# Kernel optimization log

Hardware: AMD Instinct MI355X
Metric: run time of the kernel (lower is better)

## Reference

```python
import jax, jax.numpy as jnp
import numpy as np

S, B, C, H, E = 4096, 2, 256, 8, 131072
CC = C // H


def setup_inputs() -> dict:
    key = jax.random.key(0)
    ks = jax.random.split(key, 12)
    sc = 0.02
    inp = {
        "x": jax.random.normal(ks[0], (S, B, C), jnp.float32),
        "q_id": jax.random.randint(ks[1], (E,), 0, S, jnp.int32),
        "k_id": jax.random.randint(ks[2], (E,), 0, S, jnp.int32),
        "Wq": jax.random.normal(ks[3], (C, C), jnp.float32) * sc,
        "bq": jnp.zeros((C,), jnp.float32),
        "Wk": jax.random.normal(ks[4], (C, C), jnp.float32) * sc,
        "bk": jnp.zeros((C,), jnp.float32),
        "Wv": jax.random.normal(ks[5], (C, C), jnp.float32) * sc,
        "bv": jnp.zeros((C,), jnp.float32),
        "Wx": jax.random.normal(ks[6], (C, C), jnp.float32) * sc,
        "bx": jnp.zeros((C,), jnp.float32),
    }
    return inp


def reference(x, q_id, k_id, Wq, bq, Wk, bk, Wv, bv, Wx, bx):
    s, b, c = x.shape
    cc = c // H
    # qkv projections (torch Linear: x @ W.T + b)
    q = (x @ Wq.T + bq).reshape(s, b, H, cc)
    k = (x @ Wk.T + bk).reshape(s, b, H, cc)
    v = (x @ Wv.T + bv).reshape(s, b, H, cc)
    # per-edge scores: gather along sequence axis by edge ids
    qk = jnp.einsum('ebhc,ebhc->ebh', q[q_id], k[k_id])[..., None]  # [E,b,h,1]
    qk = qk / jnp.sqrt(jnp.asarray(cc, x.dtype))
    eqk = jnp.exp(qk - jnp.max(qk))  # global max, as in original
    # scatter-add softmax normalizer and weighted sum over edges
    d = jnp.zeros((s, b, H, 1), x.dtype).at[q_id].add(eqk)
    out = jnp.zeros((s, b, H, cc), x.dtype).at[q_id].add(eqk * v[k_id])
    out = (out / d).reshape(s, b, c)
    return out @ Wx.T + bx
```

## Files before the change

### kernel.cpp

```cpp
#include <hip/hip_runtime.h>

constexpr int S_  = 4096;
constexpr int B_  = 2;
constexpr int C_  = 256;
constexpr int H_  = 8;
constexpr int E_  = 131072;
constexpr int CC_ = 32;
constexpr int MR  = S_ * B_;

typedef __attribute__((ext_vector_type(8))) short bf16x8_t;
typedef __attribute__((ext_vector_type(4))) float f32x4_t;

__device__ __forceinline__ unsigned short f2bf(float f) {
    unsigned int u = __float_as_uint(f);
    u += 0x7fffu + ((u >> 16) & 1u);
    return (unsigned short)(u >> 16);
}
__device__ __forceinline__ float bflo(unsigned int u) { return __uint_as_float(u << 16); }
__device__ __forceinline__ float bfhi(unsigned int u) { return __uint_as_float(u & 0xffff0000u); }

__device__ __forceinline__ void cast8(const float* __restrict__ src, unsigned short* __restrict__ dst, int i) {
    const float4* s = (const float4*)src + (size_t)i * 2;
    float4 a = s[0], b = s[1];
    uint4 o;
    o.x = (unsigned)f2bf(a.x) | ((unsigned)f2bf(a.y) << 16);
    o.y = (unsigned)f2bf(a.z) | ((unsigned)f2bf(a.w) << 16);
    o.z = (unsigned)f2bf(b.x) | ((unsigned)f2bf(b.y) << 16);
    o.w = (unsigned)f2bf(b.z) | ((unsigned)f2bf(b.w) << 16);
    *((uint4*)dst + i) = o;
}


__global__ __launch_bounds__(256) void prep_kernel(
        const int* __restrict__ q_id, int* __restrict__ count,
        const float* __restrict__ x, unsigned short* __restrict__ xb,
        const float* __restrict__ Wq, const float* __restrict__ Wk,
        const float* __restrict__ Wv, const float* __restrict__ Wx,
        unsigned short* __restrict__ Wb) {
    const int bid = blockIdx.x, tid = threadIdx.x;
    if (bid < 512) {
        atomicAdd(&count[q_id[bid * 256 + tid]], 1);
    } else if (bid < 1536) {
        cast8(x, xb, (bid - 512) * 256 + tid);
    } else {
        int idx = bid - 1536;
        int z = idx >> 5;
        const float* src = (z == 0) ? Wq : (z == 1) ? Wk : (z == 2) ? Wv : Wx;
        cast8(src, Wb + (size_t)z * (C_ * C_), (idx & 31) * 256 + tid);
    }
}


__global__ __launch_bounds__(1024) void scan_kernel(const int* __restrict__ count,
                                                    int* __restrict__ base,
                                                    int* __restrict__ cursor) {
    __shared__ int wsums[16];
    const int t = threadIdx.x, lane = t & 63, w = t >> 6;
    int c0 = count[4 * t + 0], c1 = count[4 * t + 1];
    int c2 = count[4 * t + 2], c3 = count[4 * t + 3];
    int tsum = c0 + c1 + c2 + c3;
    int x = tsum;
#pragma unroll
    for (int off = 1; off < 64; off <<= 1) {
        int y = __shfl_up(x, off);
        if (lane >= off) x += y;
    }
    if (lane == 63) wsums[w] = x;
    __syncthreads();
    if (t == 0) {
        int run = 0;
#pragma unroll
        for (int i = 0; i < 16; ++i) { int v = wsums[i]; wsums[i] = run; run += v; }
        base[S_] = run;
    }
    __syncthreads();
    int excl = x - tsum + wsums[w];
    int b0 = excl, b1 = b0 + c0, b2 = b1 + c1, b3 = b2 + c2;
    base[4 * t + 0] = b0; base[4 * t + 1] = b1;
    base[4 * t + 2] = b2; base[4 * t + 3] = b3;
    cursor[4 * t + 0] = b0; cursor[4 * t + 1] = b1;
    cursor[4 * t + 2] = b2; cursor[4 * t + 3] = b3;
}


__global__ __launch_bounds__(256) void scatter_qkv_kernel(
        const int* __restrict__ q_id, const int* __restrict__ k_id,
        int* __restrict__ cursor, int* __restrict__ koff_sorted,
        const unsigned short* __restrict__ xb, const unsigned short* __restrict__ Wb,
        const float* __restrict__ bq, const float* __restrict__ bk, const float* __restrict__ bv,
        unsigned short* __restrict__ qb, unsigned short* __restrict__ kvb) {
    __shared__ __align__(16) unsigned short As[64][264];
    const int bid = blockIdx.x, tid = threadIdx.x;
    if (bid >= 512) {
        int e = (bid - 512) * 256 + tid;
        int pos = atomicAdd(&cursor[q_id[e]], 1);
        koff_sorted[pos] = k_id[e] << 10;
        return;
    }
    const int nb = bid & 3, mg = bid >> 2;
    const int lane = tid & 63, wave = tid >> 6;
    const int l16 = lane & 15, quad = lane >> 4;
    const int colz = (nb << 6) + (wave << 4);

    bf16x8_t breg[3][8];
#pragma unroll
    for (int z = 0; z < 3; ++z) {
        const unsigned short* Wrow = Wb + (size_t)z * (C_ * C_) + (size_t)(colz + l16) * C_;
#pragma unroll
        for (int ks = 0; ks < 8; ++ks)
            breg[z][ks] = *(const bf16x8_t*)(Wrow + ks * 32 + quad * 8);
    }
    const float bc0 = bq[colz + l16];
    const float bc1 = bk[colz + l16];
    const float bc2 = bv[colz + l16];

    const int mbase = mg * 64;
#pragma unroll
    for (int it = 0; it < 8; ++it) {
        int l = it * 256 + tid;
        int r = l >> 5, cc = (l & 31) << 3;
        *(uint4*)&As[r][cc] = *(const uint4*)&xb[(size_t)(mbase + r) * C_ + cc];
    }
    __syncthreads();

#pragma unroll
    for (int mt = 0; mt < 4; ++mt) {
        bf16x8_t a[8];
#pragma unroll
        for (int ks = 0; ks < 8; ++ks)
            a[ks] = *(const bf16x8_t*)&As[mt * 16 + l16][ks * 32 + quad * 8];
        const int row0 = mbase + mt * 16 + quad * 4;
        {
            f32x4_t acc = {0.f, 0.f, 0.f, 0.f};
#pragma unroll
            for (int ks = 0; ks < 8; ++ks)
                acc = __builtin_amdgcn_mfma_f32_16x16x32_bf16(a[ks], breg[0][ks], acc, 0, 0, 0);
#pragma unroll
            for (int r = 0; r < 4; ++r)
                qb[(size_t)(row0 + r) * 256 + colz + l16] = f2bf(acc[r] + bc0);
        }
        {
            f32x4_t acc = {0.f, 0.f, 0.f, 0.f};
#pragma unroll
            for (int ks = 0; ks < 8; ++ks)
                acc = __builtin_amdgcn_mfma_f32_16x16x32_bf16(a[ks], breg[1][ks], acc, 0, 0, 0);
#pragma unroll
            for (int r = 0; r < 4; ++r)
                kvb[(size_t)(row0 + r) * 512 + colz + l16] = f2bf(acc[r] + bc1);
        }
        {
            f32x4_t acc = {0.f, 0.f, 0.f, 0.f};
#pragma unroll
            for (int ks = 0; ks < 8; ++ks)
                acc = __builtin_amdgcn_mfma_f32_16x16x32_bf16(a[ks], breg[2][ks], acc, 0, 0, 0);
#pragma unroll
            for (int r = 0; r < 4; ++r)
                kvb[(size_t)(row0 + r) * 512 + 256 + colz + l16] = f2bf(acc[r] + bc2);
        }
    }
}


__global__ __launch_bounds__(256) void attn_edge(
        const unsigned short* __restrict__ qb, const unsigned short* __restrict__ kvb,
        const int* __restrict__ base, const int* __restrict__ koff,
        unsigned short* __restrict__ attnb) {
    __shared__ float red[2][64][9];
    const int lane = threadIdx.x & 63;
    const int wave = threadIdx.x >> 6;
    const int rw = wave >> 1, part = wave & 1;
    const int s = blockIdx.x * 2 + rw;
    const int half = lane >> 5, hl = lane & 31;
    const int e0 = __builtin_amdgcn_readfirstlane(base[s]);
    const int e1 = __builtin_amdgcn_readfirstlane(base[s + 1]);

    const uint4 qq = *((const uint4*)(qb + (size_t)(s * 2 + half) * C_) + hl);
    const float q0 = bflo(qq.x), q1 = bfhi(qq.x), q2 = bflo(qq.y), q3 = bfhi(qq.y);
    const float q4 = bflo(qq.z), q5 = bfhi(qq.z), q6 = bflo(qq.w), q7 = bfhi(qq.w);

    float a0 = 0.f, a1 = 0.f, a2 = 0.f, a3 = 0.f, a4 = 0.f, a5 = 0.f, a6 = 0.f, a7 = 0.f;
    float wsum = 0.f;
    const float scale = 0.17677669529663687f;

    auto edge = [&](const uint4& kk, const uint4& vv) {
        float p = q0 * bflo(kk.x) + q1 * bfhi(kk.x)
                + q2 * bflo(kk.y) + q3 * bfhi(kk.y)
                + q4 * bflo(kk.z) + q5 * bfhi(kk.z)
                + q6 * bflo(kk.w) + q7 * bfhi(kk.w);
        p += __shfl_xor(p, 1);
        p += __shfl_xor(p, 2);
        const float w = __expf(p * scale);
        a0 = fmaf(w, bflo(vv.x), a0); a1 = fmaf(w, bfhi(vv.x), a1);
        a2 = fmaf(w, bflo(vv.y), a2); a3 = fmaf(w, bfhi(vv.y), a3);
        a4 = fmaf(w, bflo(vv.z), a4); a5 = fmaf(w, bfhi(vv.z), a5);
        a6 = fmaf(w, bflo(vv.w), a6); a7 = fmaf(w, bfhi(vv.w), a7);
        wsum += w;
    };
    auto fetch = [&](int my, int t, uint4& kk, uint4& vv) {
        int o = __builtin_amdgcn_readlane(my, part + 2 * t);
        const uint4* p = (const uint4*)(kvb + o + half * 512);
        kk = p[hl]; vv = p[32 + hl];
    };

    for (int b0 = e0; b0 < e1; b0 += 64) {
        const int m = min(64, e1 - b0);
        const int my = koff[b0 + ((lane < m) ? lane : 0)];
        const int nm = (m > part) ? ((m - part + 1) >> 1) : 0;
        uint4 k0 = {}, v0 = {}, k1 = {}, v1 = {};
        uint4 k2 = {}, v2 = {}, k3 = {}, v3 = {};
        if (nm > 0) fetch(my, 0, k0, v0);
        if (nm > 1) fetch(my, 1, k1, v1);
        if (nm > 2) fetch(my, 2, k2, v2);
        if (nm > 3) fetch(my, 3, k3, v3);
        int t = 0;
        for (; t + 7 < nm; t += 4) {
            edge(k0, v0); fetch(my, t + 4, k0, v0);
            edge(k1, v1); fetch(my, t + 5, k1, v1);
            edge(k2, v2); fetch(my, t + 6, k2, v2);
            edge(k3, v3); fetch(my, t + 7, k3, v3);
        }
        const int rem = nm - t;
        if (rem > 0) { edge(k0, v0); if (rem > 4) fetch(my, t + 4, k0, v0); }
        if (rem > 1) { edge(k1, v1); if (rem > 5) fetch(my, t + 5, k1, v1); }
        if (rem > 2) { edge(k2, v2); if (rem > 6) fetch(my, t + 6, k2, v2); }
        if (rem > 3) edge(k3, v3);
        if (rem > 4) edge(k0, v0);
        if (rem > 5) edge(k1, v1);
        if (rem > 6) edge(k2, v2);
    }

    if (part == 1) {
        float* r = red[rw][lane];
        r[0] = a0; r[1] = a1; r[2] = a2; r[3] = a3;
        r[4] = a4; r[5] = a5; r[6] = a6; r[7] = a7; r[8] = wsum;
    }
    __syncthreads();
    if (part == 0) {
        const float* r = red[rw][lane];
        a0 += r[0]; a1 += r[1]; a2 += r[2]; a3 += r[3];
        a4 += r[4]; a5 += r[5]; a6 += r[6]; a7 += r[7]; wsum += r[8];
        const float inv = 1.0f / wsum;
        uint4 o;
        o.x = (unsigned)f2bf(a0 * inv) | ((unsigned)f2bf(a1 * inv) << 16);
        o.y = (unsigned)f2bf(a2 * inv) | ((unsigned)f2bf(a3 * inv) << 16);
        o.z = (unsigned)f2bf(a4 * inv) | ((unsigned)f2bf(a5 * inv) << 16);
        o.w = (unsigned)f2bf(a6 * inv) | ((unsigned)f2bf(a7 * inv) << 16);
        *((uint4*)(attnb + (size_t)(s * 2 + half) * C_) + hl) = o;
    }
}


__global__ __launch_bounds__(256) void gemm_proj(
        const unsigned short* __restrict__ attnb, const unsigned short* __restrict__ Wxb,
        const float* __restrict__ bx, float* __restrict__ out) {
    __shared__ __align__(16) unsigned short As[64][264];
    const int tid = threadIdx.x;
    const int nb = blockIdx.x & 3, mg = blockIdx.x >> 2;
    const int lane = tid & 63, wave = tid >> 6;
    const int l16 = lane & 15, quad = lane >> 4;
    const int colz = (nb << 6) + (wave << 4);

    const unsigned short* Wrow = Wxb + (size_t)(colz + l16) * C_;
    bf16x8_t breg[8];
#pragma unroll
    for (int ks = 0; ks < 8; ++ks)
        breg[ks] = *(const bf16x8_t*)(Wrow + ks * 32 + quad * 8);
    const float bcol = bx[colz + l16];
    const int ocol = colz + l16;

    const int mbase = mg * 64;
#pragma unroll
    for (int it = 0; it < 8; ++it) {
        int l = it * 256 + tid;
        int r = l >> 5, cc = (l & 31) << 3;
        *(uint4*)&As[r][cc] = *(const uint4*)&attnb[(size_t)(mbase + r) * C_ + cc];
    }
    __syncthreads();
#pragma unroll
    for (int mt = 0; mt < 4; ++mt) {
        f32x4_t acc = {0.f, 0.f, 0.f, 0.f};
#pragma unroll
        for (int ks = 0; ks < 8; ++ks) {
            bf16x8_t a = *(const bf16x8_t*)&As[mt * 16 + l16][ks * 32 + quad * 8];
            acc = __builtin_amdgcn_mfma_f32_16x16x32_bf16(a, breg[ks], acc, 0, 0, 0);
        }
        const int row0 = mbase + mt * 16 + quad * 4;
#pragma unroll
        for (int r = 0; r < 4; ++r)
            out[(size_t)(row0 + r) * C_ + ocol] = acc[r] + bcol;
    }
}


extern "C" void kernel_launch(void* const* d_in, const int* in_sizes, int n_in,
                              void* d_out, int out_size, void* d_ws, size_t ws_size,
                              hipStream_t stream) {
    const float* x  = (const float*)d_in[0];
    const int* q_id = (const int*)d_in[1];
    const int* k_id = (const int*)d_in[2];
    const float* Wq = (const float*)d_in[3];
    const float* bq = (const float*)d_in[4];
    const float* Wk = (const float*)d_in[5];
    const float* bk = (const float*)d_in[6];
    const float* Wv = (const float*)d_in[7];
    const float* bv = (const float*)d_in[8];
    const float* Wx = (const float*)d_in[9];
    const float* bx = (const float*)d_in[10];
    float* out = (float*)d_out;

    char* ws = (char*)d_ws;
    unsigned short* xb    = (unsigned short*)ws;                 ws += (size_t)MR * C_ * 2;
    unsigned short* qb    = (unsigned short*)ws;                 ws += (size_t)MR * C_ * 2;
    unsigned short* kvb   = (unsigned short*)ws;                 ws += (size_t)MR * 512 * 2;
    unsigned short* attnb = (unsigned short*)ws;                 ws += (size_t)MR * C_ * 2;
    unsigned short* Wb    = (unsigned short*)ws;                 ws += (size_t)4 * C_ * C_ * 2;
    int* count       = (int*)ws;                                 ws += S_ * 4;
    int* base        = (int*)ws;                                 ws += (S_ + 1) * 4;
    int* cursor      = (int*)ws;                                 ws += S_ * 4;
    int* koff_sorted = (int*)ws;

    hipMemsetAsync(count, 0, S_ * sizeof(int), stream);
    prep_kernel<<<1664, 256, 0, stream>>>(q_id, count, x, xb, Wq, Wk, Wv, Wx, Wb);
    scan_kernel<<<1, 1024, 0, stream>>>(count, base, cursor);
    scatter_qkv_kernel<<<1024, 256, 0, stream>>>(q_id, k_id, cursor, koff_sorted,
                                                 xb, Wb, bq, bk, bv, qb, kvb);
    attn_edge<<<S_ / 2, 256, 0, stream>>>(qb, kvb, base, koff_sorted, attnb);
    gemm_proj<<<512, 256, 0, stream>>>(attnb, Wb + (size_t)3 * C_ * C_, bx, out);
}
```

Before: 145.0 us.

## Fuse all stages into one persistent kernel with software grid barriers

Replaces the five separate kernel launches (prep, scan, scatter+QKV GEMM, edge attention, output projection) with a single 512-block persistent kernel that separates phases with atomic-counter grid barriers. The aim is to remove launch gaps and per-kernel tail effects between the short stages. The attention phase also changes from two waves splitting each row's edges and reducing through shared memory to one wave per row. The design depends on all 512 blocks being co-resident (launch bounds allow 2 blocks per CU), and each phase has less parallelism than before, with the single-wave-per-row attention possibly lengthening the critical path.

```diff
diff --git a/kernel.cpp b/kernel.cpp
--- a/kernel.cpp
+++ b/kernel.cpp
@@ -5,8 +5,8 @@
 constexpr int C_  = 256;
 constexpr int H_  = 8;
 constexpr int E_  = 131072;
-constexpr int CC_ = 32;
 constexpr int MR  = S_ * B_;
+constexpr int NB  = 512;
 
 typedef __attribute__((ext_vector_type(8))) short bf16x8_t;
 typedef __attribute__((ext_vector_type(4))) float f32x4_t;
@@ -30,264 +30,233 @@
     *((uint4*)dst + i) = o;
 }
 
-
-__global__ __launch_bounds__(256) void prep_kernel(
-        const int* __restrict__ q_id, int* __restrict__ count,
-        const float* __restrict__ x, unsigned short* __restrict__ xb,
-        const float* __restrict__ Wq, const float* __restrict__ Wk,
-        const float* __restrict__ Wv, const float* __restrict__ Wx,
-        unsigned short* __restrict__ Wb) {
-    const int bid = blockIdx.x, tid = threadIdx.x;
-    if (bid < 512) {
-        atomicAdd(&count[q_id[bid * 256 + tid]], 1);
-    } else if (bid < 1536) {
-        cast8(x, xb, (bid - 512) * 256 + tid);
-    } else {
-        int idx = bid - 1536;
-        int z = idx >> 5;
-        const float* src = (z == 0) ? Wq : (z == 1) ? Wk : (z == 2) ? Wv : Wx;
-        cast8(src, Wb + (size_t)z * (C_ * C_), (idx & 31) * 256 + tid);
-    }
-}
-
-
-__global__ __launch_bounds__(1024) void scan_kernel(const int* __restrict__ count,
-                                                    int* __restrict__ base,
-                                                    int* __restrict__ cursor) {
-    __shared__ int wsums[16];
-    const int t = threadIdx.x, lane = t & 63, w = t >> 6;
-    int c0 = count[4 * t + 0], c1 = count[4 * t + 1];
-    int c2 = count[4 * t + 2], c3 = count[4 * t + 3];
-    int tsum = c0 + c1 + c2 + c3;
-    int x = tsum;
-#pragma unroll
-    for (int off = 1; off < 64; off <<= 1) {
-        int y = __shfl_up(x, off);
-        if (lane >= off) x += y;
-    }
-    if (lane == 63) wsums[w] = x;
+__device__ __forceinline__ void gbar(int* bar, int target) {
     __syncthreads();
-    if (t == 0) {
-        int run = 0;
-#pragma unroll
-        for (int i = 0; i < 16; ++i) { int v = wsums[i]; wsums[i] = run; run += v; }
-        base[S_] = run;
+    if (threadIdx.x == 0) {
+        __threadfence();
+        atomicAdd(bar, 1);
+        while (atomicAdd(bar, 0) < target)
+            __builtin_amdgcn_s_sleep(2);
+        __threadfence();
     }
     __syncthreads();
-    int excl = x - tsum + wsums[w];
-    int b0 = excl, b1 = b0 + c0, b2 = b1 + c1, b3 = b2 + c2;
-    base[4 * t + 0] = b0; base[4 * t + 1] = b1;
-    base[4 * t + 2] = b2; base[4 * t + 3] = b3;
-    cursor[4 * t + 0] = b0; cursor[4 * t + 1] = b1;
-    cursor[4 * t + 2] = b2; cursor[4 * t + 3] = b3;
-}
-
-
-__global__ __launch_bounds__(256) void scatter_qkv_kernel(
-        const int* __restrict__ q_id, const int* __restrict__ k_id,
-        int* __restrict__ cursor, int* __restrict__ koff_sorted,
-        const unsigned short* __restrict__ xb, const unsigned short* __restrict__ Wb,
-        const float* __restrict__ bq, const float* __restrict__ bk, const float* __restrict__ bv,
-        unsigned short* __restrict__ qb, unsigned short* __restrict__ kvb) {
+}
+
+__global__ __launch_bounds__(256, 2) void fused_kernel(
+        const float* __restrict__ x, const int* __restrict__ q_id, const int* __restrict__ k_id,
+        const float* __restrict__ Wq, const float* __restrict__ bq,
+        const float* __restrict__ Wk, const float* __restrict__ bk,
+        const float* __restrict__ Wv, const float* __restrict__ bv,
+        const float* __restrict__ Wx, const float* __restrict__ bx,
+        unsigned short* __restrict__ xb, unsigned short* __restrict__ qb,
+        unsigned short* __restrict__ kvb, unsigned short* __restrict__ attnb,
+        unsigned short* __restrict__ Wb,
+        int* __restrict__ count, int* bar, int* __restrict__ base,
+        int* __restrict__ cursor, int* __restrict__ koff,
+        float* __restrict__ out) {
     __shared__ __align__(16) unsigned short As[64][264];
     const int bid = blockIdx.x, tid = threadIdx.x;
-    if (bid >= 512) {
-        int e = (bid - 512) * 256 + tid;
-        int pos = atomicAdd(&cursor[q_id[e]], 1);
-        koff_sorted[pos] = k_id[e] << 10;
-        return;
-    }
-    const int nb = bid & 3, mg = bid >> 2;
+    const int gid = bid * 256 + tid;
     const int lane = tid & 63, wave = tid >> 6;
     const int l16 = lane & 15, quad = lane >> 4;
-    const int colz = (nb << 6) + (wave << 4);
-
-    bf16x8_t breg[3][8];
-#pragma unroll
-    for (int z = 0; z < 3; ++z) {
-        const unsigned short* Wrow = Wb + (size_t)z * (C_ * C_) + (size_t)(colz + l16) * C_;
+
+    cast8(x, xb, gid);
+    cast8(x, xb, gid + 131072);
+    if (gid < 32768) {
+        int z = gid >> 13, i = gid & 8191;
+        const float* src = (z == 0) ? Wq : (z == 1) ? Wk : (z == 2) ? Wv : Wx;
+        cast8(src, Wb + (size_t)z * (C_ * C_), i);
+    }
+    atomicAdd(&count[q_id[gid]], 1);
+    gbar(bar, NB);
+
+    if (bid == 0) {
+        const int4* cp = (const int4*)count;
+        int4 c0 = cp[tid * 4 + 0], c1 = cp[tid * 4 + 1];
+        int4 c2 = cp[tid * 4 + 2], c3 = cp[tid * 4 + 3];
+        int tsum = c0.x + c0.y + c0.z + c0.w + c1.x + c1.y + c1.z + c1.w
+                 + c2.x + c2.y + c2.z + c2.w + c3.x + c3.y + c3.z + c3.w;
+        int incl = tsum;
+        const int w = tid >> 6;
+#pragma unroll
+        for (int off = 1; off < 64; off <<= 1) {
+            int y = __shfl_up(incl, off);
+            if (lane >= off) incl += y;
+        }
+        int* wsums = (int*)As;
+        if (lane == 63) wsums[w] = incl;
+        __syncthreads();
+        int ws0 = wsums[0], ws1 = wsums[1], ws2 = wsums[2], ws3 = wsums[3];
+        __syncthreads();
+        if (tid == 0) base[S_] = ws0 + ws1 + ws2 + ws3;
+        int woff = (w > 0 ? ws0 : 0) + (w > 1 ? ws1 : 0) + (w > 2 ? ws2 : 0);
+        int run = woff + incl - tsum;
+        int idx = tid * 16;
+#define EMIT(V) { base[idx] = run; cursor[idx] = run; run += (V); ++idx; }
+        EMIT(c0.x) EMIT(c0.y) EMIT(c0.z) EMIT(c0.w)
+        EMIT(c1.x) EMIT(c1.y) EMIT(c1.z) EMIT(c1.w)
+        EMIT(c2.x) EMIT(c2.y) EMIT(c2.z) EMIT(c2.w)
+        EMIT(c3.x) EMIT(c3.y) EMIT(c3.z) EMIT(c3.w)
+#undef EMIT
+    }
+    for (int u = bid; u < 1024; u += NB) {
+        const int nb = u & 3, mg = u >> 2;
+        const int mbase = mg * 32;
+        __syncthreads();
+#pragma unroll
+        for (int it = 0; it < 4; ++it) {
+            int l = it * 256 + tid;
+            int r = l >> 5, cc = (l & 31) << 3;
+            *(uint4*)&As[r][cc] = *(const uint4*)&xb[(size_t)(mbase + r) * C_ + cc];
+        }
+        __syncthreads();
+        const int colz = (nb << 6) + (wave << 4);
+#pragma unroll
+        for (int z = 0; z < 3; ++z) {
+            const unsigned short* Wrow = Wb + (size_t)z * (C_ * C_) + (size_t)(colz + l16) * C_;
+            bf16x8_t breg[8];
+#pragma unroll
+            for (int ks = 0; ks < 8; ++ks)
+                breg[ks] = *(const bf16x8_t*)(Wrow + ks * 32 + quad * 8);
+            const float* bias = (z == 0) ? bq : (z == 1) ? bk : bv;
+            const float bcol = bias[colz + l16];
+#pragma unroll
+            for (int mt = 0; mt < 2; ++mt) {
+                f32x4_t acc = {0.f, 0.f, 0.f, 0.f};
+#pragma unroll
+                for (int ks = 0; ks < 8; ++ks) {
+                    bf16x8_t a = *(const bf16x8_t*)&As[mt * 16 + l16][ks * 32 + quad * 8];
+                    acc = __builtin_amdgcn_mfma_f32_16x16x32_bf16(a, breg[ks], acc, 0, 0, 0);
+                }
+                const int row0 = mbase + mt * 16 + quad * 4;
+                if (z == 0) {
+#pragma unroll
+                    for (int r = 0; r < 4; ++r)
+                        qb[(size_t)(row0 + r) * 256 + colz + l16] = f2bf(acc[r] + bcol);
+                } else if (z == 1) {
+#pragma unroll
+                    for (int r = 0; r < 4; ++r)
+                        kvb[(size_t)(row0 + r) * 512 + colz + l16] = f2bf(acc[r] + bcol);
+                } else {
+#pragma unroll
+                    for (int r = 0; r < 4; ++r)
+                        kvb[(size_t)(row0 + r) * 512 + 256 + colz + l16] = f2bf(acc[r] + bcol);
+                }
+            }
+        }
+    }
+    gbar(bar, 2 * NB);
+
+    {
+        int pos = atomicAdd(&cursor[q_id[gid]], 1);
+        koff[pos] = k_id[gid] << 10;
+    }
+    gbar(bar, 3 * NB);
+
+    {
+        const int half = lane >> 5, hl = lane & 31;
+        const float scale = 0.17677669529663687f;
+#pragma unroll
+        for (int it = 0; it < 2; ++it) {
+            const int s = (bid << 3) + (it << 2) + wave;
+            const int e0 = __builtin_amdgcn_readfirstlane(base[s]);
+            const int e1 = __builtin_amdgcn_readfirstlane(base[s + 1]);
+
+            const uint4 qq = *((const uint4*)(qb + (size_t)(s * 2 + half) * C_) + hl);
+            const float q0 = bflo(qq.x), q1 = bfhi(qq.x), q2 = bflo(qq.y), q3 = bfhi(qq.y);
+            const float q4 = bflo(qq.z), q5 = bfhi(qq.z), q6 = bflo(qq.w), q7 = bfhi(qq.w);
+
+            float a0 = 0.f, a1 = 0.f, a2 = 0.f, a3 = 0.f;
+            float a4 = 0.f, a5 = 0.f, a6 = 0.f, a7 = 0.f;
+            float wsum = 0.f;
+
+            auto edge = [&](const uint4& kk, const uint4& vv) {
+                float p = q0 * bflo(kk.x) + q1 * bfhi(kk.x)
+                        + q2 * bflo(kk.y) + q3 * bfhi(kk.y)
+                        + q4 * bflo(kk.z) + q5 * bfhi(kk.z)
+                        + q6 * bflo(kk.w) + q7 * bfhi(kk.w);
+                p += __shfl_xor(p, 1);
+                p += __shfl_xor(p, 2);
+                const float w = __expf(p * scale);
+                a0 = fmaf(w, bflo(vv.x), a0); a1 = fmaf(w, bfhi(vv.x), a1);
+                a2 = fmaf(w, bflo(vv.y), a2); a3 = fmaf(w, bfhi(vv.y), a3);
+                a4 = fmaf(w, bflo(vv.z), a4); a5 = fmaf(w, bfhi(vv.z), a5);
+                a6 = fmaf(w, bflo(vv.w), a6); a7 = fmaf(w, bfhi(vv.w), a7);
+                wsum += w;
+            };
+            auto fetch = [&](int my, int t, uint4& kk, uint4& vv) {
+                int o = __builtin_amdgcn_readlane(my, t);
+                const uint4* p = (const uint4*)(kvb + o + half * 512);
+                kk = p[hl]; vv = p[32 + hl];
+            };
+
+            for (int b0 = e0; b0 < e1; b0 += 64) {
+                const int m = min(64, e1 - b0);
+                const int my = koff[b0 + ((lane < m) ? lane : 0)];
+                uint4 k0 = {}, v0 = {}, k1 = {}, v1 = {};
+                uint4 k2 = {}, v2 = {}, k3 = {}, v3 = {};
+                if (m > 0) fetch(my, 0, k0, v0);
+                if (m > 1) fetch(my, 1, k1, v1);
+                if (m > 2) fetch(my, 2, k2, v2);
+                if (m > 3) fetch(my, 3, k3, v3);
+                int t = 0;
+                for (; t + 7 < m; t += 4) {
+                    edge(k0, v0); fetch(my, t + 4, k0, v0);
+                    edge(k1, v1); fetch(my, t + 5, k1, v1);
+                    edge(k2, v2); fetch(my, t + 6, k2, v2);
+                    edge(k3, v3); fetch(my, t + 7, k3, v3);
+                }
+                const int rem = m - t;
+                if (rem > 0) { edge(k0, v0); if (rem > 4) fetch(my, t + 4, k0, v0); }
+                if (rem > 1) { edge(k1, v1); if (rem > 5) fetch(my, t + 5, k1, v1); }
+                if (rem > 2) { edge(k2, v2); if (rem > 6) fetch(my, t + 6, k2, v2); }
+                if (rem > 3) edge(k3, v3);
+                if (rem > 4) edge(k0, v0);
+                if (rem > 5) edge(k1, v1);
+                if (rem > 6) edge(k2, v2);
+            }
+
+            const float inv = 1.0f / wsum;
+            uint4 o;
+            o.x = (unsigned)f2bf(a0 * inv) | ((unsigned)f2bf(a1 * inv) << 16);
+            o.y = (unsigned)f2bf(a2 * inv) | ((unsigned)f2bf(a3 * inv) << 16);
+            o.z = (unsigned)f2bf(a4 * inv) | ((unsigned)f2bf(a5 * inv) << 16);
+            o.w = (unsigned)f2bf(a6 * inv) | ((unsigned)f2bf(a7 * inv) << 16);
+            *((uint4*)(attnb + (size_t)(s * 2 + half) * C_) + hl) = o;
+        }
+    }
+    gbar(bar, 4 * NB);
+
+    {
+        const int nbp = bid & 3, mgp = bid >> 2;
+        const int mbase = mgp * 64;
+#pragma unroll
+        for (int it = 0; it < 8; ++it) {
+            int l = it * 256 + tid;
+            int r = l >> 5, cc = (l & 31) << 3;
+            *(uint4*)&As[r][cc] = *(const uint4*)&attnb[(size_t)(mbase + r) * C_ + cc];
+        }
+        __syncthreads();
+        const int colz = (nbp << 6) + (wave << 4);
+        const unsigned short* Wrow = Wb + (size_t)3 * (C_ * C_) + (size_t)(colz + l16) * C_;
+        bf16x8_t breg[8];
 #pragma unroll
         for (int ks = 0; ks < 8; ++ks)
-            breg[z][ks] = *(const bf16x8_t*)(Wrow + ks * 32 + quad * 8);
-    }
-    const float bc0 = bq[colz + l16];
-    const float bc1 = bk[colz + l16];
-    const float bc2 = bv[colz + l16];
-
-    const int mbase = mg * 64;
-#pragma unroll
-    for (int it = 0; it < 8; ++it) {
-        int l = it * 256 + tid;
-        int r = l >> 5, cc = (l & 31) << 3;
-        *(uint4*)&As[r][cc] = *(const uint4*)&xb[(size_t)(mbase + r) * C_ + cc];
-    }
-    __syncthreads();
-
-#pragma unroll
-    for (int mt = 0; mt < 4; ++mt) {
-        bf16x8_t a[8];
-#pragma unroll
-        for (int ks = 0; ks < 8; ++ks)
-            a[ks] = *(const bf16x8_t*)&As[mt * 16 + l16][ks * 32 + quad * 8];
-        const int row0 = mbase + mt * 16 + quad * 4;
-        {
+            breg[ks] = *(const bf16x8_t*)(Wrow + ks * 32 + quad * 8);
+        const float bcol = bx[colz + l16];
+#pragma unroll
+        for (int mt = 0; mt < 4; ++mt) {
             f32x4_t acc = {0.f, 0.f, 0.f, 0.f};
 #pragma unroll
-            for (int ks = 0; ks < 8; ++ks)
-                acc = __builtin_amdgcn_mfma_f32_16x16x32_bf16(a[ks], breg[0][ks], acc, 0, 0, 0);
+            for (int ks = 0; ks < 8; ++ks) {
+                bf16x8_t a = *(const bf16x8_t*)&As[mt * 16 + l16][ks * 32 + quad * 8];
+                acc = __builtin_amdgcn_mfma_f32_16x16x32_bf16(a, breg[ks], acc, 0, 0, 0);
+            }
+            const int row0 = mbase + mt * 16 + quad * 4;
 #pragma unroll
             for (int r = 0; r < 4; ++r)
-                qb[(size_t)(row0 + r) * 256 + colz + l16] = f2bf(acc[r] + bc0);
-        }
-        {
-            f32x4_t acc = {0.f, 0.f, 0.f, 0.f};
-#pragma unroll
-            for (int ks = 0; ks < 8; ++ks)
-                acc = __builtin_amdgcn_mfma_f32_16x16x32_bf16(a[ks], breg[1][ks], acc, 0, 0, 0);
-#pragma unroll
-            for (int r = 0; r < 4; ++r)
-                kvb[(size_t)(row0 + r) * 512 + colz + l16] = f2bf(acc[r] + bc1);
-        }
-        {
-            f32x4_t acc = {0.f, 0.f, 0.f, 0.f};
-#pragma unroll
-            for (int ks = 0; ks < 8; ++ks)
-                acc = __builtin_amdgcn_mfma_f32_16x16x32_bf16(a[ks], breg[2][ks], acc, 0, 0, 0);
-#pragma unroll
-            for (int r = 0; r < 4; ++r)
-                kvb[(size_t)(row0 + r) * 512 + 256 + colz + l16] = f2bf(acc[r] + bc2);
-        }
-    }
-}
-
-
-__global__ __launch_bounds__(256) void attn_edge(
-        const unsigned short* __restrict__ qb, const unsigned short* __restrict__ kvb,
-        const int* __restrict__ base, const int* __restrict__ koff,
-        unsigned short* __restrict__ attnb) {
-    __shared__ float red[2][64][9];
-    const int lane = threadIdx.x & 63;
-    const int wave = threadIdx.x >> 6;
-    const int rw = wave >> 1, part = wave & 1;
-    const int s = blockIdx.x * 2 + rw;
-    const int half = lane >> 5, hl = lane & 31;
-    const int e0 = __builtin_amdgcn_readfirstlane(base[s]);
-    const int e1 = __builtin_amdgcn_readfirstlane(base[s + 1]);
-
-    const uint4 qq = *((const uint4*)(qb + (size_t)(s * 2 + half) * C_) + hl);
-    const float q0 = bflo(qq.x), q1 = bfhi(qq.x), q2 = bflo(qq.y), q3 = bfhi(qq.y);
-    const float q4 = bflo(qq.z), q5 = bfhi(qq.z), q6 = bflo(qq.w), q7 = bfhi(qq.w);
-
-    float a0 = 0.f, a1 = 0.f, a2 = 0.f, a3 = 0.f, a4 = 0.f, a5 = 0.f, a6 = 0.f, a7 = 0.f;
-    float wsum = 0.f;
-    const float scale = 0.17677669529663687f;
-
-    auto edge = [&](const uint4& kk, const uint4& vv) {
-        float p = q0 * bflo(kk.x) + q1 * bfhi(kk.x)
-                + q2 * bflo(kk.y) + q3 * bfhi(kk.y)
-                + q4 * bflo(kk.z) + q5 * bfhi(kk.z)
-                + q6 * bflo(kk.w) + q7 * bfhi(kk.w);
-        p += __shfl_xor(p, 1);
-        p += __shfl_xor(p, 2);
-        const float w = __expf(p * scale);
-        a0 = fmaf(w, bflo(vv.x), a0); a1 = fmaf(w, bfhi(vv.x), a1);
-        a2 = fmaf(w, bflo(vv.y), a2); a3 = fmaf(w, bfhi(vv.y), a3);
-        a4 = fmaf(w, bflo(vv.z), a4); a5 = fmaf(w, bfhi(vv.z), a5);
-        a6 = fmaf(w, bflo(vv.w), a6); a7 = fmaf(w, bfhi(vv.w), a7);
-        wsum += w;
-    };
-    auto fetch = [&](int my, int t, uint4& kk, uint4& vv) {
-        int o = __builtin_amdgcn_readlane(my, part + 2 * t);
-        const uint4* p = (const uint4*)(kvb + o + half * 512);
-        kk = p[hl]; vv = p[32 + hl];
-    };
-
-    for (int b0 = e0; b0 < e1; b0 += 64) {
-        const int m = min(64, e1 - b0);
-        const int my = koff[b0 + ((lane < m) ? lane : 0)];
-        const int nm = (m > part) ? ((m - part + 1) >> 1) : 0;
-        uint4 k0 = {}, v0 = {}, k1 = {}, v1 = {};
-        uint4 k2 = {}, v2 = {}, k3 = {}, v3 = {};
-        if (nm > 0) fetch(my, 0, k0, v0);
-        if (nm > 1) fetch(my, 1, k1, v1);
-        if (nm > 2) fetch(my, 2, k2, v2);
-        if (nm > 3) fetch(my, 3, k3, v3);
-        int t = 0;
-        for (; t + 7 < nm; t += 4) {
-            edge(k0, v0); fetch(my, t + 4, k0, v0);
-            edge(k1, v1); fetch(my, t + 5, k1, v1);
-            edge(k2, v2); fetch(my, t + 6, k2, v2);
-            edge(k3, v3); fetch(my, t + 7, k3, v3);
-        }
-        const int rem = nm - t;
-        if (rem > 0) { edge(k0, v0); if (rem > 4) fetch(my, t + 4, k0, v0); }
-        if (rem > 1) { edge(k1, v1); if (rem > 5) fetch(my, t + 5, k1, v1); }
-        if (rem > 2) { edge(k2, v2); if (rem > 6) fetch(my, t + 6, k2, v2); }
-        if (rem > 3) edge(k3, v3);
-        if (rem > 4) edge(k0, v0);
-        if (rem > 5) edge(k1, v1);
-        if (rem > 6) edge(k2, v2);
-    }
-
-    if (part == 1) {
-        float* r = red[rw][lane];
-        r[0] = a0; r[1] = a1; r[2] = a2; r[3] = a3;
-        r[4] = a4; r[5] = a5; r[6] = a6; r[7] = a7; r[8] = wsum;
-    }
-    __syncthreads();
-    if (part == 0) {
-        const float* r = red[rw][lane];
-        a0 += r[0]; a1 += r[1]; a2 += r[2]; a3 += r[3];
-        a4 += r[4]; a5 += r[5]; a6 += r[6]; a7 += r[7]; wsum += r[8];
-        const float inv = 1.0f / wsum;
-        uint4 o;
-        o.x = (unsigned)f2bf(a0 * inv) | ((unsigned)f2bf(a1 * inv) << 16);
-        o.y = (unsigned)f2bf(a2 * inv) | ((unsigned)f2bf(a3 * inv) << 16);
-        o.z = (unsigned)f2bf(a4 * inv) | ((unsigned)f2bf(a5 * inv) << 16);
-        o.w = (unsigned)f2bf(a6 * inv) | ((unsigned)f2bf(a7 * inv) << 16);
-        *((uint4*)(attnb + (size_t)(s * 2 + half) * C_) + hl) = o;
-    }
-}
-
-
-__global__ __launch_bounds__(256) void gemm_proj(
-        const unsigned short* __restrict__ attnb, const unsigned short* __restrict__ Wxb,
-        const float* __restrict__ bx, float* __restrict__ out) {
-    __shared__ __align__(16) unsigned short As[64][264];
-    const int tid = threadIdx.x;
-    const int nb = blockIdx.x & 3, mg = blockIdx.x >> 2;
-    const int lane = tid & 63, wave = tid >> 6;
-    const int l16 = lane & 15, quad = lane >> 4;
-    const int colz = (nb << 6) + (wave << 4);
-
-    const unsigned short* Wrow = Wxb + (size_t)(colz + l16) * C_;
-    bf16x8_t breg[8];
-#pragma unroll
-    for (int ks = 0; ks < 8; ++ks)
-        breg[ks] = *(const bf16x8_t*)(Wrow + ks * 32 + quad * 8);
-    const float bcol = bx[colz + l16];
-    const int ocol = colz + l16;
-
-    const int mbase = mg * 64;
-#pragma unroll
-    for (int it = 0; it < 8; ++it) {
-        int l = it * 256 + tid;
-        int r = l >> 5, cc = (l & 31) << 3;
-        *(uint4*)&As[r][cc] = *(const uint4*)&attnb[(size_t)(mbase + r) * C_ + cc];
-    }
-    __syncthreads();
-#pragma unroll
-    for (int mt = 0; mt < 4; ++mt) {
-        f32x4_t acc = {0.f, 0.f, 0.f, 0.f};
-#pragma unroll
-        for (int ks = 0; ks < 8; ++ks) {
-            bf16x8_t a = *(const bf16x8_t*)&As[mt * 16 + l16][ks * 32 + quad * 8];
-            acc = __builtin_amdgcn_mfma_f32_16x16x32_bf16(a, breg[ks], acc, 0, 0, 0);
-        }
-        const int row0 = mbase + mt * 16 + quad * 4;
-#pragma unroll
-        for (int r = 0; r < 4; ++r)
-            out[(size_t)(row0 + r) * C_ + ocol] = acc[r] + bcol;
+                out[(size_t)(row0 + r) * C_ + colz + l16] = acc[r] + bcol;
+        }
     }
 }
 
@@ -309,21 +278,19 @@
     float* out = (float*)d_out;
 
     char* ws = (char*)d_ws;
-    unsigned short* xb    = (unsigned short*)ws;                 ws += (size_t)MR * C_ * 2;
-    unsigned short* qb    = (unsigned short*)ws;                 ws += (size_t)MR * C_ * 2;
-    unsigned short* kvb   = (unsigned short*)ws;                 ws += (size_t)MR * 512 * 2;
-    unsigned short* attnb = (unsigned short*)ws;                 ws += (size_t)MR * C_ * 2;
-    unsigned short* Wb    = (unsigned short*)ws;                 ws += (size_t)4 * C_ * C_ * 2;
-    int* count       = (int*)ws;                                 ws += S_ * 4;
-    int* base        = (int*)ws;                                 ws += (S_ + 1) * 4;
-    int* cursor      = (int*)ws;                                 ws += S_ * 4;
+    unsigned short* xb    = (unsigned short*)ws;   ws += (size_t)MR * C_ * 2;
+    unsigned short* qb    = (unsigned short*)ws;   ws += (size_t)MR * C_ * 2;
+    unsigned short* kvb   = (unsigned short*)ws;   ws += (size_t)MR * 512 * 2;
+    unsigned short* attnb = (unsigned short*)ws;   ws += (size_t)MR * C_ * 2;
+    unsigned short* Wb    = (unsigned short*)ws;   ws += (size_t)4 * C_ * C_ * 2;
+    int* count = (int*)ws;                         ws += S_ * 4;
+    int* bar   = (int*)ws;                         ws += 8 * 4;
+    int* base  = (int*)ws;                         ws += (S_ + 1) * 4;
+    int* cursor = (int*)ws;                        ws += S_ * 4;
     int* koff_sorted = (int*)ws;
 
-    hipMemsetAsync(count, 0, S_ * sizeof(int), stream);
-    prep_kernel<<<1664, 256, 0, stream>>>(q_id, count, x, xb, Wq, Wk, Wv, Wx, Wb);
-    scan_kernel<<<1, 1024, 0, stream>>>(count, base, cursor);
-    scatter_qkv_kernel<<<1024, 256, 0, stream>>>(q_id, k_id, cursor, koff_sorted,
-                                                 xb, Wb, bq, bk, bv, qb, kvb);
-    attn_edge<<<S_ / 2, 256, 0, stream>>>(qb, kvb, base, koff_sorted, attnb);
-    gemm_proj<<<512, 256, 0, stream>>>(attnb, Wb + (size_t)3 * C_ * C_, bx, out);
-}
+    hipMemsetAsync(count, 0, (S_ + 8) * sizeof(int), stream);
+    fused_kernel<<<NB, 256, 0, stream>>>(x, q_id, k_id, Wq, bq, Wk, bk, Wv, bv, Wx, bx,
+                                         xb, qb, kvb, attnb, Wb,
+                                         count, bar, base, cursor, koff_sorted, out);
+}
```

After: 361.6 us. +149.3%, slower.

## Fuse scan into prep via last-block pattern, cast x inline, bucket edges by key half

Applied to the files above, without the earlier changes.

The separate scan kernel is folded into prep_kernel: the last block to finish, detected with an atomic counter, performs the prefix sum. The x fp32-to-bf16 cast is moved into the QKV GEMM's shared-memory load, which removes the xb buffer and one full pass over memory. Edges are now bucketed by query and by which half of the key range they hit, so attn_edge walks two segments per row with better K/V locality. This removes a kernel launch and a memory round-trip, at the cost of a serialized tail scan in the last prep block and an extra segment loop.

```diff
diff --git a/kernel.cpp b/kernel.cpp
--- a/kernel.cpp
+++ b/kernel.cpp
@@ -5,8 +5,8 @@
 constexpr int C_  = 256;
 constexpr int H_  = 8;
 constexpr int E_  = 131072;
-constexpr int CC_ = 32;
 constexpr int MR  = S_ * B_;
+constexpr int PREP_BLOCKS = 640;
 
 typedef __attribute__((ext_vector_type(8))) short bf16x8_t;
 typedef __attribute__((ext_vector_type(4))) float f32x4_t;
@@ -32,69 +32,79 @@
 
 
 __global__ __launch_bounds__(256) void prep_kernel(
-        const int* __restrict__ q_id, int* __restrict__ count,
-        const float* __restrict__ x, unsigned short* __restrict__ xb,
+        const int* __restrict__ q_id, const int* __restrict__ k_id,
         const float* __restrict__ Wq, const float* __restrict__ Wk,
         const float* __restrict__ Wv, const float* __restrict__ Wx,
-        unsigned short* __restrict__ Wb) {
+        unsigned short* __restrict__ Wb,
+        int* __restrict__ count, int* done,
+        int* __restrict__ base, int* __restrict__ cursor) {
     const int bid = blockIdx.x, tid = threadIdx.x;
     if (bid < 512) {
-        atomicAdd(&count[q_id[bid * 256 + tid]], 1);
-    } else if (bid < 1536) {
-        cast8(x, xb, (bid - 512) * 256 + tid);
+        int e = bid * 256 + tid;
+        int q = q_id[e], k = k_id[e];
+        atomicAdd(&count[q + ((k >> 11) << 12)], 1);
     } else {
-        int idx = bid - 1536;
+        int idx = bid - 512;
         int z = idx >> 5;
         const float* src = (z == 0) ? Wq : (z == 1) ? Wk : (z == 2) ? Wv : Wx;
         cast8(src, Wb + (size_t)z * (C_ * C_), (idx & 31) * 256 + tid);
     }
-}
-
-
-__global__ __launch_bounds__(1024) void scan_kernel(const int* __restrict__ count,
-                                                    int* __restrict__ base,
-                                                    int* __restrict__ cursor) {
-    __shared__ int wsums[16];
-    const int t = threadIdx.x, lane = t & 63, w = t >> 6;
-    int c0 = count[4 * t + 0], c1 = count[4 * t + 1];
-    int c2 = count[4 * t + 2], c3 = count[4 * t + 3];
-    int tsum = c0 + c1 + c2 + c3;
-    int x = tsum;
+
+    __shared__ int amLast;
+    __syncthreads();
+    if (tid == 0) {
+        int d = __hip_atomic_fetch_add(done, 1, __ATOMIC_RELAXED, __HIP_MEMORY_SCOPE_AGENT);
+        amLast = (d == PREP_BLOCKS - 1);
+    }
+    __syncthreads();
+    if (!amLast) return;
+    __builtin_amdgcn_fence(__ATOMIC_ACQUIRE, "agent");
+
+    const int lane = tid & 63, w = tid >> 6;
+    const int4* cp = (const int4*)count;
+    int4 c[8];
+#pragma unroll
+    for (int j = 0; j < 8; ++j) c[j] = cp[tid * 8 + j];
+    int tsum = 0;
+#pragma unroll
+    for (int j = 0; j < 8; ++j) tsum += c[j].x + c[j].y + c[j].z + c[j].w;
+    int incl = tsum;
 #pragma unroll
     for (int off = 1; off < 64; off <<= 1) {
-        int y = __shfl_up(x, off);
-        if (lane >= off) x += y;
-    }
-    if (lane == 63) wsums[w] = x;
-    __syncthreads();
-    if (t == 0) {
-        int run = 0;
-#pragma unroll
-        for (int i = 0; i < 16; ++i) { int v = wsums[i]; wsums[i] = run; run += v; }
-        base[S_] = run;
-    }
-    __syncthreads();
-    int excl = x - tsum + wsums[w];
-    int b0 = excl, b1 = b0 + c0, b2 = b1 + c1, b3 = b2 + c2;
-    base[4 * t + 0] = b0; base[4 * t + 1] = b1;
-    base[4 * t + 2] = b2; base[4 * t + 3] = b3;
-    cursor[4 * t + 0] = b0; cursor[4 * t + 1] = b1;
-    cursor[4 * t + 2] = b2; cursor[4 * t + 3] = b3;
+        int y = __shfl_up(incl, off);
+        if (lane >= off) incl += y;
+    }
+    __shared__ int wsums[4];
+    if (lane == 63) wsums[w] = incl;
+    __syncthreads();
+    int ws0 = wsums[0], ws1 = wsums[1], ws2 = wsums[2];
+    if (tid == 0) base[2 * S_] = E_;
+    int woff = (w > 0 ? ws0 : 0) + (w > 1 ? ws1 : 0) + (w > 2 ? ws2 : 0);
+    int run = woff + incl - tsum;
+    int idx = tid * 32;
+#define EMIT(V) { base[idx] = run; cursor[idx] = run; run += (V); ++idx; }
+#pragma unroll
+    for (int j = 0; j < 8; ++j) {
+        EMIT(c[j].x) EMIT(c[j].y) EMIT(c[j].z) EMIT(c[j].w)
+    }
+#undef EMIT
 }
 
 
 __global__ __launch_bounds__(256) void scatter_qkv_kernel(
+        const float* __restrict__ x,
         const int* __restrict__ q_id, const int* __restrict__ k_id,
-        int* __restrict__ cursor, int* __restrict__ koff_sorted,
-        const unsigned short* __restrict__ xb, const unsigned short* __restrict__ Wb,
+        int* __restrict__ cursor, int* __restrict__ koff,
+        const unsigned short* __restrict__ Wb,
         const float* __restrict__ bq, const float* __restrict__ bk, const float* __restrict__ bv,
         unsigned short* __restrict__ qb, unsigned short* __restrict__ kvb) {
     __shared__ __align__(16) unsigned short As[64][264];
     const int bid = blockIdx.x, tid = threadIdx.x;
     if (bid >= 512) {
         int e = (bid - 512) * 256 + tid;
-        int pos = atomicAdd(&cursor[q_id[e]], 1);
-        koff_sorted[pos] = k_id[e] << 10;
+        int q = q_id[e], k = k_id[e];
+        int pos = atomicAdd(&cursor[q + ((k >> 11) << 12)], 1);
+        koff[pos] = k << 10;
         return;
     }
     const int nb = bid & 3, mg = bid >> 2;
@@ -117,9 +127,16 @@
     const int mbase = mg * 64;
 #pragma unroll
     for (int it = 0; it < 8; ++it) {
-        int l = it * 256 + tid;
-        int r = l >> 5, cc = (l & 31) << 3;
-        *(uint4*)&As[r][cc] = *(const uint4*)&xb[(size_t)(mbase + r) * C_ + cc];
+        int u = it * 256 + tid;
+        int r = u >> 5, cc = (u & 31) << 3;
+        const float4* s = (const float4*)(x + (size_t)(mbase + r) * C_ + cc);
+        float4 a = s[0], b = s[1];
+        uint4 o;
+        o.x = (unsigned)f2bf(a.x) | ((unsigned)f2bf(a.y) << 16);
+        o.y = (unsigned)f2bf(a.z) | ((unsigned)f2bf(a.w) << 16);
+        o.z = (unsigned)f2bf(b.x) | ((unsigned)f2bf(b.y) << 16);
+        o.w = (unsigned)f2bf(b.z) | ((unsigned)f2bf(b.w) << 16);
+        *(uint4*)&As[r][cc] = o;
     }
     __syncthreads();
 
@@ -171,8 +188,6 @@
     const int rw = wave >> 1, part = wave & 1;
     const int s = blockIdx.x * 2 + rw;
     const int half = lane >> 5, hl = lane & 31;
-    const int e0 = __builtin_amdgcn_readfirstlane(base[s]);
-    const int e1 = __builtin_amdgcn_readfirstlane(base[s + 1]);
 
     const uint4 qq = *((const uint4*)(qb + (size_t)(s * 2 + half) * C_) + hl);
     const float q0 = bflo(qq.x), q1 = bfhi(qq.x), q2 = bflo(qq.y), q3 = bfhi(qq.y);
@@ -202,31 +217,37 @@
         kk = p[hl]; vv = p[32 + hl];
     };
 
-    for (int b0 = e0; b0 < e1; b0 += 64) {
-        const int m = min(64, e1 - b0);
-        const int my = koff[b0 + ((lane < m) ? lane : 0)];
-        const int nm = (m > part) ? ((m - part + 1) >> 1) : 0;
-        uint4 k0 = {}, v0 = {}, k1 = {}, v1 = {};
-        uint4 k2 = {}, v2 = {}, k3 = {}, v3 = {};
-        if (nm > 0) fetch(my, 0, k0, v0);
-        if (nm > 1) fetch(my, 1, k1, v1);
-        if (nm > 2) fetch(my, 2, k2, v2);
-        if (nm > 3) fetch(my, 3, k3, v3);
-        int t = 0;
-        for (; t + 7 < nm; t += 4) {
-            edge(k0, v0); fetch(my, t + 4, k0, v0);
-            edge(k1, v1); fetch(my, t + 5, k1, v1);
-            edge(k2, v2); fetch(my, t + 6, k2, v2);
-            edge(k3, v3); fetch(my, t + 7, k3, v3);
-        }
-        const int rem = nm - t;
-        if (rem > 0) { edge(k0, v0); if (rem > 4) fetch(my, t + 4, k0, v0); }
-        if (rem > 1) { edge(k1, v1); if (rem > 5) fetch(my, t + 5, k1, v1); }
-        if (rem > 2) { edge(k2, v2); if (rem > 6) fetch(my, t + 6, k2, v2); }
-        if (rem > 3) edge(k3, v3);
-        if (rem > 4) edge(k0, v0);
-        if (rem > 5) edge(k1, v1);
-        if (rem > 6) edge(k2, v2);
+#pragma unroll
+    for (int seg = 0; seg < 2; ++seg) {
+        const int cb = seg * S_ + s;
+        const int e0 = __builtin_amdgcn_readfirstlane(base[cb]);
+        const int e1 = __builtin_amdgcn_readfirstlane(base[cb + 1]);
+        for (int b0 = e0; b0 < e1; b0 += 64) {
+            const int m = min(64, e1 - b0);
+            const int my = koff[b0 + ((lane < m) ? lane : 0)];
+            const int nm = (m > part) ? ((m - part + 1) >> 1) : 0;
+            uint4 k0 = {}, v0 = {}, k1 = {}, v1 = {};
+            uint4 k2 = {}, v2 = {}, k3 = {}, v3 = {};
+            if (nm > 0) fetch(my, 0, k0, v0);
+            if (nm > 1) fetch(my, 1, k1, v1);
+            if (nm > 2) fetch(my, 2, k2, v2);
+            if (nm > 3) fetch(my, 3, k3, v3);
+            int t = 0;
+            for (; t + 7 < nm; t += 4) {
+                edge(k0, v0); fetch(my, t + 4, k0, v0);
+                edge(k1, v1); fetch(my, t + 5, k1, v1);
+                edge(k2, v2); fetch(my, t + 6, k2, v2);
+                edge(k3, v3); fetch(my, t + 7, k3, v3);
+            }
+            const int rem = nm - t;
+            if (rem > 0) { edge(k0, v0); if (rem > 4) fetch(my, t + 4, k0, v0); }
+            if (rem > 1) { edge(k1, v1); if (rem > 5) fetch(my, t + 5, k1, v1); }
+            if (rem > 2) { edge(k2, v2); if (rem > 6) fetch(my, t + 6, k2, v2); }
+            if (rem > 3) edge(k3, v3);
+            if (rem > 4) edge(k0, v0);
+            if (rem > 5) edge(k1, v1);
+            if (rem > 6) edge(k2, v2);
+        }
     }
 
     if (part == 1) {
@@ -266,7 +287,6 @@
     for (int ks = 0; ks < 8; ++ks)
         breg[ks] = *(const bf16x8_t*)(Wrow + ks * 32 + quad * 8);
     const float bcol = bx[colz + l16];
-    const int ocol = colz + l16;
 
     const int mbase = mg * 64;
 #pragma unroll
@@ -287,7 +307,7 @@
         const int row0 = mbase + mt * 16 + quad * 4;
 #pragma unroll
         for (int r = 0; r < 4; ++r)
-            out[(size_t)(row0 + r) * C_ + ocol] = acc[r] + bcol;
+            out[(size_t)(row0 + r) * C_ + colz + l16] = acc[r] + bcol;
     }
 }
 
@@ -309,21 +329,21 @@
     float* out = (float*)d_out;
 
     char* ws = (char*)d_ws;
-    unsigned short* xb    = (unsigned short*)ws;                 ws += (size_t)MR * C_ * 2;
-    unsigned short* qb    = (unsigned short*)ws;                 ws += (size_t)MR * C_ * 2;
-    unsigned short* kvb   = (unsigned short*)ws;                 ws += (size_t)MR * 512 * 2;
-    unsigned short* attnb = (unsigned short*)ws;                 ws += (size_t)MR * C_ * 2;
-    unsigned short* Wb    = (unsigned short*)ws;                 ws += (size_t)4 * C_ * C_ * 2;
-    int* count       = (int*)ws;                                 ws += S_ * 4;
-    int* base        = (int*)ws;                                 ws += (S_ + 1) * 4;
-    int* cursor      = (int*)ws;                                 ws += S_ * 4;
+    unsigned short* qb    = (unsigned short*)ws;   ws += (size_t)MR * C_ * 2;
+    unsigned short* kvb   = (unsigned short*)ws;   ws += (size_t)MR * 512 * 2;
+    unsigned short* attnb = (unsigned short*)ws;   ws += (size_t)MR * C_ * 2;
+    unsigned short* Wb    = (unsigned short*)ws;   ws += (size_t)4 * C_ * C_ * 2;
+    int* count = (int*)ws;                         ws += 2 * S_ * 4;
+    int* done  = (int*)ws;                         ws += 16 * 4;
+    int* base  = (int*)ws;                         ws += (2 * S_ + 1) * 4;
+    int* cursor = (int*)ws;                        ws += 2 * S_ * 4;
     int* koff_sorted = (int*)ws;
 
-    hipMemsetAsync(count, 0, S_ * sizeof(int), stream);
-    prep_kernel<<<1664, 256, 0, stream>>>(q_id, count, x, xb, Wq, Wk, Wv, Wx, Wb);
-    scan_kernel<<<1, 1024, 0, stream>>>(count, base, cursor);
-    scatter_qkv_kernel<<<1024, 256, 0, stream>>>(q_id, k_id, cursor, koff_sorted,
-                                                 xb, Wb, bq, bk, bv, qb, kvb);
+    hipMemsetAsync(count, 0, (2 * S_ + 16) * sizeof(int), stream);
+    prep_kernel<<<PREP_BLOCKS, 256, 0, stream>>>(q_id, k_id, Wq, Wk, Wv, Wx, Wb,
+                                                 count, done, base, cursor);
+    scatter_qkv_kernel<<<1024, 256, 0, stream>>>(x, q_id, k_id, cursor, koff_sorted,
+                                                 Wb, bq, bk, bv, qb, kvb);
     attn_edge<<<S_ / 2, 256, 0, stream>>>(qb, kvb, base, koff_sorted, attnb);
     gemm_proj<<<512, 256, 0, stream>>>(attnb, Wb + (size_t)3 * C_ * C_, bx, out);
 }
```

New measurement: 144.0 us. About the same (-0.7%).
